# Optimization experiments

Measured on AMD Instinct MI355X. Metric: run time of the kernel, lower is better.

The kernel has to match this reference:

```python
import jax, jax.numpy as jnp
import numpy as np

B, T, I, H, O = 64, 1024, 512, 1024, 512


def setup_inputs() -> dict:
    key = jax.random.key(0)
    ks = jax.random.split(key, 8)
    s_in = 1.0 / np.sqrt(I)
    s_g = 1.0 / np.sqrt(2 * H)
    s_o = 1.0 / np.sqrt(H)
    return {
        "inputs": jax.random.normal(ks[0], (B, T, I), dtype=jnp.float32),
        "h": jax.random.normal(ks[1], (B, H), dtype=jnp.float32),
        "W_in": jax.random.uniform(ks[2], (H, I), minval=-s_in, maxval=s_in, dtype=jnp.float32),
        "b_in": jax.random.uniform(ks[3], (H,), minval=-s_in, maxval=s_in, dtype=jnp.float32),
        "W_gate": jax.random.uniform(ks[4], (H, 2 * H), minval=-s_g, maxval=s_g, dtype=jnp.float32),
        "b_gate": jax.random.uniform(ks[5], (H,), minval=-s_g, maxval=s_g, dtype=jnp.float32),
        "W_out": jax.random.uniform(ks[6], (O, H), minval=-s_o, maxval=s_o, dtype=jnp.float32),
        "b_out": jax.random.uniform(ks[7], (O,), minval=-s_o, maxval=s_o, dtype=jnp.float32),
    }


def reference(inputs, h, W_in, b_in, W_gate, b_gate, W_out, b_out):
    # input_layer has no time dependence -> compute for all steps at once.
    # z: [T, B, H]
    z = jnp.einsum("bti,hi->tbh", inputs, W_in) + b_in
    # gate_layer acts on cat([h, z_t]); split its weight accordingly.
    Wg_h = W_gate[:, :H]   # [H, H] applied to h
    Wg_z = W_gate[:, H:]   # [H, H] applied to z_t

    def step(h_prev, z_t):
        u = jax.nn.sigmoid(h_prev @ Wg_h.T + z_t @ Wg_z.T + b_gate)
        h_new = u * h_prev + (1.0 - u) * z_t
        return h_new, h_new

    h_final, hs = jax.lax.scan(step, h, z)  # hs: [T, B, H]
    # output_layer applied to every hidden state, vectorized over time.
    outs = jnp.einsum("tbh,oh->bto", hs, W_out) + b_out  # [B, T, O]
    return (outs, h_final)
```

## Files before the change

### kernel.cpp

```cpp
#include <hip/hip_runtime.h>

#define B_ 64
#define T_ 1024
#define I_ 512
#define H_ 1024
#define O_ 512
#define BH (B_*H_)

using short8 = __attribute__((ext_vector_type(8))) short;
using f32x4  = __attribute__((ext_vector_type(4))) float;

__device__ __forceinline__ unsigned short f2b(float f) {
  unsigned int u = __float_as_uint(f);
  u = (u + 0x7fffu + ((u >> 16) & 1u)) >> 16;
  return (unsigned short)u;
}
__device__ __forceinline__ float b2f(unsigned short h) {
  return __uint_as_float(((unsigned int)h) << 16);
}

#define WAIT_VM0() __builtin_amdgcn_s_waitcnt(0x0F70)

__device__ __forceinline__ void glds16(const ushort* g, ushort* l) {
  __builtin_amdgcn_global_load_lds(
      (const __attribute__((address_space(1))) void*)g,
      (__attribute__((address_space(3))) void*)l, 16, 0, 0);
}

__global__ void cast4_kernel(const float* __restrict__ src, ushort* __restrict__ dst, int n4) {
  int i = blockIdx.x * 256 + threadIdx.x;
  if (i >= n4) return;
  float4 v = ((const float4*)src)[i];
  ushort4 o; o.x = f2b(v.x); o.y = f2b(v.y); o.z = f2b(v.z); o.w = f2b(v.w);
  ((ushort4*)dst)[i] = o;
}

__global__ void cast_gate_kernel(const float* __restrict__ src, ushort* __restrict__ dst) {
  int i = blockIdx.x * 256 + threadIdx.x;
  int row = i >> 8, k4 = (i & 255) << 2;
  float4 v = *(const float4*)(src + (size_t)row * 2048 + 1024 + k4);
  ushort4 o; o.x = f2b(v.x); o.y = f2b(v.y); o.z = f2b(v.z); o.w = f2b(v.w);
  ((ushort4*)dst)[((size_t)row << 8) + (k4 >> 2)] = o;
}

__global__ __launch_bounds__(256)
void cast_inputs_kernel(const float* __restrict__ src, ushort* __restrict__ dst) {
  int i = blockIdx.x * 256 + threadIdx.x;
  int rp = i >> 7;
  int e4 = (i & 127) << 2;
  int b = rp >> 10, t = rp & 1023;
  float4 v = *(const float4*)(src + ((size_t)rp << 9) + e4);
  ushort4 o; o.x = f2b(v.x); o.y = f2b(v.y); o.z = f2b(v.z); o.w = f2b(v.w);
  *(ushort4*)(dst + (((size_t)(t << 6) + b) << 9) + e4) = o;
}

__global__ __launch_bounds__(256)
void gemm_bt_tiled(const ushort* __restrict__ A, const ushort* __restrict__ W,
                   const float* __restrict__ bias, void* __restrict__ Cout,
                   int M, int N, int K, int modeC)
{
  __shared__ __align__(16) ushort As[128 * 32];
  __shared__ __align__(16) ushort Bs[128 * 32];

  const int tid  = threadIdx.x;
  const int wave = tid >> 6, lane = tid & 63;
  const int q = lane >> 4, col = lane & 15;

  const int n0 = blockIdx.x * 128;
  const int m0 = blockIdx.y * 128;

  const int wr = (wave >> 1) * 64;
  const int wc = (wave & 1) * 64;

  const int srow = tid >> 2;
  const int skk  = (tid & 3) << 3;
  const ushort* Ag = A + (size_t)(m0 + srow) * K + skk;
  const ushort* Wg = W + (size_t)(n0 + srow) * K + skk;
  ushort* AsW = As + wave * 512;
  ushort* BsW = Bs + wave * 512;

  f32x4 acc[4][4];
  #pragma unroll
  for (int i = 0; i < 4; ++i)
    #pragma unroll
    for (int j = 0; j < 4; ++j) acc[i][j] = (f32x4){0.f, 0.f, 0.f, 0.f};

  const ushort* Asr = As + ((size_t)(wr + col) << 5) + q * 8;
  const ushort* Bsr = Bs + ((size_t)(wc + col) << 5) + q * 8;

  for (int k0 = 0; k0 < K; k0 += 32) {
    __syncthreads();
    glds16(Ag + k0,                   AsW);
    glds16(Ag + (size_t)64 * K + k0,  AsW + 2048);
    glds16(Wg + k0,                   BsW);
    glds16(Wg + (size_t)64 * K + k0,  BsW + 2048);
    __syncthreads();

    short8 af[4], bf[4];
    #pragma unroll
    for (int mt = 0; mt < 4; ++mt) af[mt] = *(const short8*)(Asr + mt * 16 * 32);
    #pragma unroll
    for (int nt = 0; nt < 4; ++nt) bf[nt] = *(const short8*)(Bsr + nt * 16 * 32);
    #pragma unroll
    for (int mt = 0; mt < 4; ++mt)
      #pragma unroll
      for (int nt = 0; nt < 4; ++nt)
        acc[mt][nt] = __builtin_amdgcn_mfma_f32_16x16x32_bf16(af[mt], bf[nt], acc[mt][nt], 0, 0, 0);
  }

  #pragma unroll
  for (int nt = 0; nt < 4; ++nt) {
    int n = n0 + wc + nt * 16 + col;
    float bv = bias[n];
    #pragma unroll
    for (int mt = 0; mt < 4; ++mt) {
      #pragma unroll
      for (int r = 0; r < 4; ++r) {
        int row = m0 + wr + mt * 16 + q * 4 + r;
        float v = acc[mt][nt][r] + bv;
        if (modeC == 0) {
          ((ushort*)Cout)[(size_t)row * N + n] = f2b(v);
        } else {
          int b = row & 63, t = row >> 6;
          ((float*)Cout)[(size_t)b * (T_ * O_) + (size_t)t * O_ + n] = v;
        }
      }
    }
  }
}

__device__ __forceinline__ void scan_step(
    int t, int g, int b0, int n0, int lane, int q, int col,
    const short8* __restrict__ wfv, ushort* __restrict__ hbuf,
    float* __restrict__ hfinal, int* __restrict__ flags,
    const float zv[4], const float av[4], float hp[4])
{
  const int fidx = (g << 6) + lane;
  for (;;) {
    int v = __hip_atomic_load(&flags[fidx], __ATOMIC_RELAXED, __HIP_MEMORY_SCOPE_AGENT);
    if (__ballot(v < t) == 0ull) break;
    __builtin_amdgcn_s_sleep(1);
  }
  __builtin_amdgcn_fence(__ATOMIC_ACQUIRE, "workgroup");

  const ushort* hrow = hbuf + (size_t)(t - 1) * BH + (size_t)(b0 + col) * H_ + q * 8;
  f32x4 acc0 = {0.f, 0.f, 0.f, 0.f}, acc1 = {0.f, 0.f, 0.f, 0.f};
  #pragma unroll
  for (int ks = 0; ks < 32; ks += 2) {
    short8 h0f = *(const short8*)(hrow + ks * 32);
    short8 h1f = *(const short8*)(hrow + (ks + 1) * 32);
    acc0 = __builtin_amdgcn_mfma_f32_16x16x32_bf16(h0f, wfv[ks * 64 + lane], acc0, 0, 0, 0);
    acc1 = __builtin_amdgcn_mfma_f32_16x16x32_bf16(h1f, wfv[(ks + 1) * 64 + lane], acc1, 0, 0, 0);
  }
  f32x4 S = acc0 + acc1;

  #pragma unroll
  for (int r = 0; r < 4; ++r) {
    int b = b0 + q * 4 + r;
    float x  = S[r] + av[r];
    float u  = 1.0f / (1.0f + __expf(-x));
    float hn = u * hp[r] + (1.0f - u) * zv[r];
    hp[r] = hn;
    unsigned int own = f2b(hn);
    unsigned int other = ((unsigned int)__shfl_xor((int)own, 1, 64)) & 0xffffu;
    if ((col & 1) == 0) {
      unsigned int dw = own | (other << 16);
      __hip_atomic_store((unsigned int*)(hbuf + (size_t)t * BH + (size_t)b * H_ + n0 + col),
                         dw, __ATOMIC_RELAXED, __HIP_MEMORY_SCOPE_AGENT);
    }
    if (t == T_) hfinal[(size_t)b * H_ + n0 + col] = hn;
  }
  WAIT_VM0();
  if (lane == 0)
    __hip_atomic_store(&flags[(g << 6) + (n0 >> 4)], t + 1,
                       __ATOMIC_RELAXED, __HIP_MEMORY_SCOPE_AGENT);
}

__global__ __launch_bounds__(64)
void scan_kernel(const ushort* __restrict__ z, const ushort* __restrict__ a,
                 ushort* __restrict__ hbuf, const float* __restrict__ Wgate,
                 const float* __restrict__ h0, float* __restrict__ hfinal,
                 int* __restrict__ flags)
{
  __shared__ __align__(16) short Wf[32 * 64 * 8];

  const int tid = threadIdx.x;
  const int member = blockIdx.x & 63;
  const int pairid = blockIdx.x >> 6;
  const int gA = pairid * 2, gB = pairid * 2 + 1;
  const int b0A = gA << 4, b0B = gB << 4;
  const int n0 = member << 4;
  const int lane = tid;
  const int q = lane >> 4, col = lane & 15;

  short8* wfv = (short8*)Wf;

  {
    const float* wsrc = Wgate + (size_t)(n0 + col) * 2048 + (q * 8);
    for (int ks = 0; ks < 32; ++ks) {
      float4 w0 = *(const float4*)(wsrc + ks * 32);
      float4 w1 = *(const float4*)(wsrc + ks * 32 + 4);
      short8 v;
      v[0] = (short)f2b(w0.x); v[1] = (short)f2b(w0.y);
      v[2] = (short)f2b(w0.z); v[3] = (short)f2b(w0.w);
      v[4] = (short)f2b(w1.x); v[5] = (short)f2b(w1.y);
      v[6] = (short)f2b(w1.z); v[7] = (short)f2b(w1.w);
      wfv[ks * 64 + lane] = v;
    }
  }

  #pragma unroll
  for (int grp = 0; grp < 2; ++grp) {
    int b0 = grp ? b0B : b0A;
    #pragma unroll
    for (int i = 0; i < 2; ++i) {
      int idx = tid + 64 * i;
      int b = b0 + (idx >> 3);
      int n = n0 + (idx & 7) * 2;
      const float* hp0 = h0 + (size_t)b * H_ + n;
      unsigned int dw = (unsigned int)f2b(hp0[0]) | ((unsigned int)f2b(hp0[1]) << 16);
      __hip_atomic_store((unsigned int*)(hbuf + (size_t)b * H_ + n), dw,
                         __ATOMIC_RELAXED, __HIP_MEMORY_SCOPE_AGENT);
    }
  }

  float hpA[4], hpB[4];
  #pragma unroll
  for (int r = 0; r < 4; ++r) {
    hpA[r] = h0[(size_t)(b0A + q * 4 + r) * H_ + n0 + col];
    hpB[r] = h0[(size_t)(b0B + q * 4 + r) * H_ + n0 + col];
  }

  WAIT_VM0();
  if (tid == 0) {
    __hip_atomic_store(&flags[(gA << 6) + member], 1, __ATOMIC_RELAXED, __HIP_MEMORY_SCOPE_AGENT);
    __hip_atomic_store(&flags[(gB << 6) + member], 1, __ATOMIC_RELAXED, __HIP_MEMORY_SCOPE_AGENT);
  }

  for (int t = 1; t <= T_; ++t) {
    float zvA[4], avA[4], zvB[4], avB[4];
    {
      const size_t baseA = (size_t)(t - 1) * BH + (size_t)(b0A + q * 4) * H_ + n0 + col;
      const size_t baseB = (size_t)(t - 1) * BH + (size_t)(b0B + q * 4) * H_ + n0 + col;
      #pragma unroll
      for (int r = 0; r < 4; ++r) {
        zvA[r] = b2f(z[baseA + (size_t)r * H_]);
        avA[r] = b2f(a[baseA + (size_t)r * H_]);
        zvB[r] = b2f(z[baseB + (size_t)r * H_]);
        avB[r] = b2f(a[baseB + (size_t)r * H_]);
      }
    }
    scan_step(t, gA, b0A, n0, lane, q, col, wfv, hbuf, hfinal, flags, zvA, avA, hpA);
    scan_step(t, gB, b0B, n0, lane, q, col, wfv, hbuf, hfinal, flags, zvB, avB, hpB);
  }
}

extern "C" void kernel_launch(void* const* d_in, const int* in_sizes, int n_in,
                              void* d_out, int out_size, void* d_ws, size_t ws_size,
                              hipStream_t stream) {
  const float* inputs = (const float*)d_in[0];
  const float* h0     = (const float*)d_in[1];
  const float* W_in   = (const float*)d_in[2];
  const float* b_in   = (const float*)d_in[3];
  const float* W_gate = (const float*)d_in[4];
  const float* b_gate = (const float*)d_in[5];
  const float* W_out  = (const float*)d_in[6];
  const float* b_out  = (const float*)d_in[7];

  char* ws = (char*)d_ws;
  ushort* Winbf  = (ushort*)(ws + 0);
  ushort* Wgzbf  = (ushort*)(ws + (1u << 20));
  ushort* Woutbf = (ushort*)(ws + 3 * (1u << 20));
  ushort* z_bf   = (ushort*)(ws + 4 * (1u << 20));
  ushort* a_bf   = (ushort*)(ws + (size_t)4 * (1u << 20) + (size_t)134217728);
  ushort* hbuf   = (ushort*)(ws + (size_t)4 * (1u << 20) + (size_t)2 * 134217728);
  int*    flags  = (int*)   (ws + (size_t)4 * (1u << 20) + (size_t)2 * 134217728 + (size_t)134348800);

  ushort* Abf = a_bf;

  hipMemsetAsync(flags, 0, 4 * 64 * sizeof(int), stream);

  cast4_kernel<<<dim3((H_ * I_ / 4 + 255) / 256), dim3(256), 0, stream>>>(W_in, Winbf, H_ * I_ / 4);
  cast4_kernel<<<dim3((O_ * H_ / 4 + 255) / 256), dim3(256), 0, stream>>>(W_out, Woutbf, O_ * H_ / 4);
  cast_gate_kernel<<<dim3(H_ * H_ / 4 / 256), dim3(256), 0, stream>>>(W_gate, Wgzbf);
  cast_inputs_kernel<<<dim3(B_ * T_ * I_ / 4 / 256), dim3(256), 0, stream>>>(inputs, Abf);

  gemm_bt_tiled<<<dim3(H_ / 128, (B_ * T_) / 128), dim3(256), 0, stream>>>(
      Abf, Winbf, b_in, (void*)z_bf, B_ * T_, H_, I_, 0);

  gemm_bt_tiled<<<dim3(H_ / 128, (B_ * T_) / 128), dim3(256), 0, stream>>>(
      z_bf, Wgzbf, b_gate, (void*)a_bf, B_ * T_, H_, H_, 0);

  {
    float* hfinal = (float*)d_out + (size_t)B_ * T_ * O_;
    const ushort* zc = z_bf; const ushort* ac = a_bf;
    ushort* hb = hbuf; const float* wg = W_gate; const float* h0c = h0;
    int* flg = flags;
    void* sargs[7] = { (void*)&zc, (void*)&ac, (void*)&hb, (void*)&wg,
                       (void*)&h0c, (void*)&hfinal, (void*)&flg };
    hipLaunchCooperativeKernel((const void*)scan_kernel, dim3(128), dim3(64), sargs, 0, stream);
  }

  gemm_bt_tiled<<<dim3(O_ / 128, (B_ * T_) / 128), dim3(256), 0, stream>>>(
      hbuf + BH, Woutbf, b_out, d_out, B_ * T_, O_, H_, 1);
}
```

Baseline: 8.404 ms.

## Map four batch groups to four waves per block in scan kernel

The recurrent scan now launches 64 blocks of 256 threads instead of 128 single-wave blocks. Each wave owns one 16-row batch group and processes it independently, where before one wave handled two groups one after the other. The waves of a block share a single LDS copy of the gate weights, loaded cooperatively, so redundant weight staging is removed. Each wave now waits only on its own group's flags, so the serial per-step chain per wave is halved. In exchange, four waves compete for one CU's resources and there are fewer blocks across the device.

```diff
diff --git a/kernel.cpp b/kernel.cpp
--- a/kernel.cpp
+++ b/kernel.cpp
@@ -176,7 +176,7 @@
                        __ATOMIC_RELAXED, __HIP_MEMORY_SCOPE_AGENT);
 }
 
-__global__ __launch_bounds__(64)
+__global__ __launch_bounds__(256)
 void scan_kernel(const ushort* __restrict__ z, const ushort* __restrict__ a,
                  ushort* __restrict__ hbuf, const float* __restrict__ Wgate,
                  const float* __restrict__ h0, float* __restrict__ hfinal,
@@ -185,19 +185,18 @@
   __shared__ __align__(16) short Wf[32 * 64 * 8];
 
   const int tid = threadIdx.x;
-  const int member = blockIdx.x & 63;
-  const int pairid = blockIdx.x >> 6;
-  const int gA = pairid * 2, gB = pairid * 2 + 1;
-  const int b0A = gA << 4, b0B = gB << 4;
+  const int member = blockIdx.x;
+  const int g = tid >> 6;
+  const int lane = tid & 63;
+  const int q = lane >> 4, col = lane & 15;
+  const int b0 = g << 4;
   const int n0 = member << 4;
-  const int lane = tid;
-  const int q = lane >> 4, col = lane & 15;
 
   short8* wfv = (short8*)Wf;
 
   {
     const float* wsrc = Wgate + (size_t)(n0 + col) * 2048 + (q * 8);
-    for (int ks = 0; ks < 32; ++ks) {
+    for (int ks = 8 * g; ks < 8 * g + 8; ++ks) {
       float4 w0 = *(const float4*)(wsrc + ks * 32);
       float4 w1 = *(const float4*)(wsrc + ks * 32 + 4);
       short8 v;
@@ -208,50 +207,37 @@
       wfv[ks * 64 + lane] = v;
     }
   }
-
-  #pragma unroll
-  for (int grp = 0; grp < 2; ++grp) {
-    int b0 = grp ? b0B : b0A;
-    #pragma unroll
-    for (int i = 0; i < 2; ++i) {
-      int idx = tid + 64 * i;
-      int b = b0 + (idx >> 3);
-      int n = n0 + (idx & 7) * 2;
-      const float* hp0 = h0 + (size_t)b * H_ + n;
-      unsigned int dw = (unsigned int)f2b(hp0[0]) | ((unsigned int)f2b(hp0[1]) << 16);
-      __hip_atomic_store((unsigned int*)(hbuf + (size_t)b * H_ + n), dw,
-                         __ATOMIC_RELAXED, __HIP_MEMORY_SCOPE_AGENT);
-    }
-  }
-
-  float hpA[4], hpB[4];
-  #pragma unroll
-  for (int r = 0; r < 4; ++r) {
-    hpA[r] = h0[(size_t)(b0A + q * 4 + r) * H_ + n0 + col];
-    hpB[r] = h0[(size_t)(b0B + q * 4 + r) * H_ + n0 + col];
-  }
+  __syncthreads();
+
+  #pragma unroll
+  for (int i = 0; i < 2; ++i) {
+    int idx = lane + 64 * i;
+    int b = b0 + (idx >> 3);
+    int n = n0 + (idx & 7) * 2;
+    const float* hp0 = h0 + (size_t)b * H_ + n;
+    unsigned int dw = (unsigned int)f2b(hp0[0]) | ((unsigned int)f2b(hp0[1]) << 16);
+    __hip_atomic_store((unsigned int*)(hbuf + (size_t)b * H_ + n), dw,
+                       __ATOMIC_RELAXED, __HIP_MEMORY_SCOPE_AGENT);
+  }
+
+  float hp[4];
+  #pragma unroll
+  for (int r = 0; r < 4; ++r)
+    hp[r] = h0[(size_t)(b0 + q * 4 + r) * H_ + n0 + col];
 
   WAIT_VM0();
-  if (tid == 0) {
-    __hip_atomic_store(&flags[(gA << 6) + member], 1, __ATOMIC_RELAXED, __HIP_MEMORY_SCOPE_AGENT);
-    __hip_atomic_store(&flags[(gB << 6) + member], 1, __ATOMIC_RELAXED, __HIP_MEMORY_SCOPE_AGENT);
-  }
+  if (lane == 0)
+    __hip_atomic_store(&flags[(g << 6) + member], 1, __ATOMIC_RELAXED, __HIP_MEMORY_SCOPE_AGENT);
 
   for (int t = 1; t <= T_; ++t) {
-    float zvA[4], avA[4], zvB[4], avB[4];
-    {
-      const size_t baseA = (size_t)(t - 1) * BH + (size_t)(b0A + q * 4) * H_ + n0 + col;
-      const size_t baseB = (size_t)(t - 1) * BH + (size_t)(b0B + q * 4) * H_ + n0 + col;
-      #pragma unroll
-      for (int r = 0; r < 4; ++r) {
-        zvA[r] = b2f(z[baseA + (size_t)r * H_]);
-        avA[r] = b2f(a[baseA + (size_t)r * H_]);
-        zvB[r] = b2f(z[baseB + (size_t)r * H_]);
-        avB[r] = b2f(a[baseB + (size_t)r * H_]);
-      }
-    }
-    scan_step(t, gA, b0A, n0, lane, q, col, wfv, hbuf, hfinal, flags, zvA, avA, hpA);
-    scan_step(t, gB, b0B, n0, lane, q, col, wfv, hbuf, hfinal, flags, zvB, avB, hpB);
+    float zv[4], av[4];
+    const size_t base = (size_t)(t - 1) * BH + (size_t)(b0 + q * 4) * H_ + n0 + col;
+    #pragma unroll
+    for (int r = 0; r < 4; ++r) {
+      zv[r] = b2f(z[base + (size_t)r * H_]);
+      av[r] = b2f(a[base + (size_t)r * H_]);
+    }
+    scan_step(t, g, b0, n0, lane, q, col, wfv, hbuf, hfinal, flags, zv, av, hp);
   }
 }
 
@@ -298,7 +284,7 @@
     int* flg = flags;
     void* sargs[7] = { (void*)&zc, (void*)&ac, (void*)&hb, (void*)&wg,
                        (void*)&h0c, (void*)&hfinal, (void*)&flg };
-    hipLaunchCooperativeKernel((const void*)scan_kernel, dim3(128), dim3(64), sargs, 0, stream);
+    hipLaunchCooperativeKernel((const void*)scan_kernel, dim3(64), dim3(256), sargs, 0, stream);
   }
 
   gemm_bt_tiled<<<dim3(O_ / 128, (B_ * T_) / 128), dim3(256), 0, stream>>>(
```

New measurement: 9.398 ms. +11.8%, slower.
